# Kernel tuning notes

Hardware: AMD Instinct MI355X
Metric: run time of the kernel (lower is better)

## Reference

```python
import jax, jax.numpy as jnp
import numpy as np

VOCAB = 100000
DIM = 128
B = 16384
CWIN = 10
K = 10
EPS = 1e-9


def setup_inputs() -> dict:
    key = jax.random.key(0)
    k1, k2, k3, k4, k5 = jax.random.split(key, 5)
    context = jax.random.randint(k1, (B, CWIN), 0, VOCAB)
    target = jax.random.randint(k2, (B,), 0, VOCAB)
    negatives = jax.random.randint(k3, (B, K), 0, VOCAB)
    in_emb = jax.random.normal(k4, (VOCAB, DIM), dtype=jnp.float32)
    out_emb = jax.random.normal(k5, (VOCAB, DIM), dtype=jnp.float32)
    return {"context": context, "target": target, "negatives": negatives,
            "in_emb": in_emb, "out_emb": out_emb}


def reference(context, target, negatives, in_emb, out_emb):
    # context: [B, C] int; target: [B] int; negatives: [B, K] int
    context_embed = in_emb[context]                      # [B, C, D]
    context_mean = jnp.mean(context_embed, axis=1)       # [B, D]
    target_embed = out_emb[target]                       # [B, D]
    neg_embed = out_emb[negatives]                       # [B, K, D]
    pos_score = jnp.sum(context_mean * target_embed, axis=1)          # [B]
    pos_loss = jnp.log(jax.nn.sigmoid(pos_score) + EPS)               # [B]
    neg_score = jnp.einsum('bkd,bd->bk', neg_embed, context_mean)     # [B, K]
    neg_loss = jnp.sum(jnp.log(jax.nn.sigmoid(-neg_score) + EPS), axis=1)  # [B]
    return -jnp.mean(pos_loss + neg_loss)
```

## Files before the change

kernel.cpp:

```cpp
#include <hip/hip_runtime.h>


#define VOCAB  100000
#define DIM    128
#define B_TOT  16384
#define CWIN   10
#define K_NEG  10
#define EPS_F  1e-9f

#define BPB    8
#define NBLK   (B_TOT / BPB)

__global__ __launch_bounds__(256, 4) void cbow_loss_kernel(
    const int*   __restrict__ context,
    const int*   __restrict__ target,
    const int*   __restrict__ negatives,
    const float* __restrict__ in_emb,
    const float* __restrict__ out_emb,
    float*       __restrict__ per_b)
{
    const int tid    = threadIdx.x;
    const int halfId = tid >> 5;
    const int sub    = tid & 31;
    const int b      = blockIdx.x * BPB + halfId;

    const float4* in4  = (const float4*)in_emb;
    const float4* out4 = (const float4*)out_emb;

    int myIdx = 0;
    {
        const int* p  = target;
        int        off = b;
        if (sub < CWIN)                 { p = context;   off = b * CWIN + sub; }
        else if (sub < 2 * CWIN)        { p = negatives; off = b * K_NEG + (sub - CWIN); }
        if (sub <= 2 * CWIN) myIdx = p[off];
    }

    float4 cr[CWIN];
#pragma unroll
    for (int c = 0; c < CWIN; ++c) {
        const int idx = __shfl(myIdx, c, 32);
        cr[c] = in4[(idx << 5) + sub];
    }
    float4 ov[K_NEG + 1];
#pragma unroll
    for (int k = 0; k <= K_NEG; ++k) {
        const int lanesrc = (k == 0) ? 2 * CWIN : (CWIN + k - 1);
        const int idx = __shfl(myIdx, lanesrc, 32);
        ov[k] = out4[(idx << 5) + sub];
    }

    float4 cm = make_float4(0.f, 0.f, 0.f, 0.f);
#pragma unroll
    for (int c = 0; c < CWIN; ++c) {
        cm.x += cr[c].x; cm.y += cr[c].y; cm.z += cr[c].z; cm.w += cr[c].w;
    }
    cm.x *= (1.0f / CWIN); cm.y *= (1.0f / CWIN);
    cm.z *= (1.0f / CWIN); cm.w *= (1.0f / CWIN);

    float s[K_NEG + 1];
#pragma unroll
    for (int k = 0; k <= K_NEG; ++k)
        s[k] = cm.x * ov[k].x + cm.y * ov[k].y + cm.z * ov[k].z + cm.w * ov[k].w;

#pragma unroll
    for (int j = 0; j <= K_NEG; ++j) {
        float x = s[j];
#pragma unroll
        for (int off = 16; off > 0; off >>= 1)
            x += __shfl_xor(x, off, 64);
        s[j] = x;
    }

    float l = __logf(1.0f / (1.0f + __expf(-s[0])) + EPS_F);
#pragma unroll
    for (int k = 1; k <= K_NEG; ++k)
        l += __logf(1.0f / (1.0f + __expf(s[k])) + EPS_F);

    if (sub == 0) per_b[b] = l;
}

__global__ __launch_bounds__(256) void finalize_kernel(
    const float* __restrict__ per_b,
    float*       __restrict__ out)
{
    const int tid  = threadIdx.x;
    const int lane = tid & 63;
    const int wave = tid >> 6;

    float x = 0.f;
#pragma unroll
    for (int j = 0; j < B_TOT / 256; ++j)
        x += per_b[tid + 256 * j];

#pragma unroll
    for (int off = 32; off > 0; off >>= 1)
        x += __shfl_xor(x, off, 64);

    __shared__ float part[4];
    if (lane == 0) part[wave] = x;
    __syncthreads();
    if (tid == 0)
        out[0] = -(part[0] + part[1] + part[2] + part[3]) * (1.0f / B_TOT);
}

extern "C" void kernel_launch(void* const* d_in, const int* in_sizes, int n_in,
                              void* d_out, int out_size, void* d_ws, size_t ws_size,
                              hipStream_t stream) {
    const int*   context   = (const int*)  d_in[0];
    const int*   target    = (const int*)  d_in[1];
    const int*   negatives = (const int*)  d_in[2];
    const float* in_emb    = (const float*)d_in[3];
    const float* out_emb   = (const float*)d_in[4];
    float*       out       = (float*)d_out;
    float*       per_b     = (float*)d_ws;

    cbow_loss_kernel<<<NBLK, 256, 0, stream>>>(
        context, target, negatives, in_emb, out_emb, per_b);
    finalize_kernel<<<1, 256, 0, stream>>>(per_b, out);
}
```

Baseline: 130.8 us.

## Fuse final reduction into main kernel via last-block atomic counter

Each block now sums its 8 per-sample losses in shared memory and writes a single partial, then increments a global atomic counter. The last block to arrive reduces all block partials and writes the final loss, resetting the counter. This removes the second kernel launch and its gap and shrinks the partials array, at the cost of an atomic plus two block barriers in every block.

```diff
diff --git a/kernel.cpp b/kernel.cpp
--- a/kernel.cpp
+++ b/kernel.cpp
@@ -11,13 +11,16 @@
 #define BPB    8
 #define NBLK   (B_TOT / BPB)
 
+__device__ unsigned int g_done = 0;
+
 __global__ __launch_bounds__(256, 4) void cbow_loss_kernel(
     const int*   __restrict__ context,
     const int*   __restrict__ target,
     const int*   __restrict__ negatives,
     const float* __restrict__ in_emb,
     const float* __restrict__ out_emb,
-    float*       __restrict__ per_b)
+    float*       __restrict__ partials,
+    float*       __restrict__ out)
 {
     const int tid    = threadIdx.x;
     const int halfId = tid >> 5;
@@ -77,31 +80,40 @@
     for (int k = 1; k <= K_NEG; ++k)
         l += __logf(1.0f / (1.0f + __expf(s[k])) + EPS_F);
 
-    if (sub == 0) per_b[b] = l;
-}
+    __shared__ float        lpart[BPB];
+    __shared__ unsigned int s_isLast;
+    if (sub == 0) lpart[halfId] = l;
+    __syncthreads();
 
-__global__ __launch_bounds__(256) void finalize_kernel(
-    const float* __restrict__ per_b,
-    float*       __restrict__ out)
-{
-    const int tid  = threadIdx.x;
-    const int lane = tid & 63;
-    const int wave = tid >> 6;
+    if (tid == 0) {
+        float p8 = 0.f;
+#pragma unroll
+        for (int i = 0; i < BPB; ++i) p8 += lpart[i];
+        partials[blockIdx.x] = p8;
+        unsigned int old = __hip_atomic_fetch_add(
+            &g_done, 1u, __ATOMIC_ACQ_REL, __HIP_MEMORY_SCOPE_AGENT);
+        if (old == NBLK - 1) __threadfence();
+        s_isLast = (old == NBLK - 1) ? 1u : 0u;
+    }
+    __syncthreads();
 
-    float x = 0.f;
+    if (s_isLast) {
+        float x = 0.f;
 #pragma unroll
-    for (int j = 0; j < B_TOT / 256; ++j)
-        x += per_b[tid + 256 * j];
-
+        for (int j = 0; j < NBLK / 256; ++j)
+            x += partials[tid + 256 * j];
 #pragma unroll
-    for (int off = 32; off > 0; off >>= 1)
-        x += __shfl_xor(x, off, 64);
-
-    __shared__ float part[4];
-    if (lane == 0) part[wave] = x;
-    __syncthreads();
-    if (tid == 0)
-        out[0] = -(part[0] + part[1] + part[2] + part[3]) * (1.0f / B_TOT);
+        for (int off = 32; off > 0; off >>= 1)
+            x += __shfl_xor(x, off, 64);
+        __shared__ float wpart[4];
+        const int lane = tid & 63, wave = tid >> 6;
+        if (lane == 0) wpart[wave] = x;
+        __syncthreads();
+        if (tid == 0) {
+            out[0] = -(wpart[0] + wpart[1] + wpart[2] + wpart[3]) * (1.0f / B_TOT);
+            g_done = 0;
+        }
+    }
 }
 
 extern "C" void kernel_launch(void* const* d_in, const int* in_sizes, int n_in,
@@ -113,9 +125,8 @@
     const float* in_emb    = (const float*)d_in[3];
     const float* out_emb   = (const float*)d_in[4];
     float*       out       = (float*)d_out;
-    float*       per_b     = (float*)d_ws;
+    float*       partials  = (float*)d_ws;
 
     cbow_loss_kernel<<<NBLK, 256, 0, stream>>>(
-        context, target, negatives, in_emb, out_emb, per_b);
-    finalize_kernel<<<1, 256, 0, stream>>>(per_b, out);
+        context, target, negatives, in_emb, out_emb, partials, out);
 }
```

New measurement: 224.0 us. 1.71x slower.
